# Optimization experiments

Hardware: AMD Instinct MI355X
Metric: run time of the kernel (lower is better)

The kernel has to match this reference:

```python
import jax, jax.numpy as jnp
import numpy as np

N = 4194304  # number of curve segments


def setup_inputs() -> dict:
    key = jax.random.key(0)
    k1, k2, k3, k4 = jax.random.split(key, 4)
    # small per-step turning angles (radians)
    vec = 0.001 * jax.random.normal(k1, (N,), dtype=jnp.float32)
    vec2 = 0.001 * jax.random.normal(k2, (N,), dtype=jnp.float32)
    the0 = jnp.asarray([np.pi / 6.0], dtype=jnp.float32)
    the02 = jnp.asarray([np.pi + np.arcsin(1.0 / 7.0)], dtype=jnp.float32)
    PS = jnp.zeros((1, 2), dtype=jnp.float32)
    PE = jnp.asarray([[100.0, 0.0]], dtype=jnp.float32)
    dl = jnp.asarray([0.001], dtype=jnp.float32)
    return {"vec": vec, "vec2": vec2, "the0": the0, "the02": the02,
            "PS": PS, "PE": PE, "dl": dl}


def _curve(start, the0, vec, dl):
    # Per-step rotation matvec recurrence pre_i = R(vec_i) @ pre_{i-1},
    # pre_0 = dl * R(the0) @ [1, 0]. Rotations compose additively, so the
    # recurrence is exactly cumulative angles + cumsum of step vectors.
    theta = the0 + jnp.cumsum(vec)                      # [n]
    steps = dl[0] * jnp.stack([jnp.cos(theta), jnp.sin(theta)], axis=-1)  # [n, 2]
    path = start[-1] + jnp.cumsum(steps, axis=0)        # [n, 2]
    return jnp.concatenate([start, path], axis=0)       # [n+1, 2]


def reference(vec, vec2, the0, the02, PS, PE, dl):
    P = _curve(PS, the0, vec, dl)
    P2 = _curve(PE, the02, vec2, dl)
    return (P, P2)
```

## Files before the change

kernel.cpp:

```cpp
#include <hip/hip_runtime.h>

#define NSEG   4194304
#define BLOCK  256
#define ITEMS  16
#define TILE   (BLOCK * ITEMS)
#define NTILES (NSEG / TILE)
#define WAVES  (BLOCK / 64)

static_assert(NSEG % TILE == 0, "tile must divide N");

__device__ __forceinline__ void combineSeg(float aT, float aC, float aS,
                                           float bT, float bC, float bS,
                                           float& oT, float& oC, float& oS) {
    float s, c;
    __sincosf(aT, &s, &c);
    oT = aT + bT;
    oC = aC + c * bC - s * bS;
    oS = aS + s * bC + c * bS;
}

__global__ __launch_bounds__(BLOCK) void k_tilesum(
        const float* __restrict__ vec, const float* __restrict__ vec2,
        float4* __restrict__ part) {
    const int c = blockIdx.y;
    const int b = blockIdx.x;
    const int t = threadIdx.x;
    const int lane = t & 63, wave = t >> 6;
    const float* __restrict__ v = c ? vec2 : vec;

    __shared__ float sW[WAVES], sRC[WAVES], sRS[WAVES];

    const float4* __restrict__ p =
        reinterpret_cast<const float4*>(v + (size_t)b * TILE) +
        (size_t)t * (ITEMS / 4);
    float vals[ITEMS];
#pragma unroll
    for (int q = 0; q < ITEMS / 4; ++q) {
        float4 a = p[q];
        vals[q * 4 + 0] = a.x; vals[q * 4 + 1] = a.y;
        vals[q * 4 + 2] = a.z; vals[q * 4 + 3] = a.w;
    }
    float tsum = 0.f;
#pragma unroll
    for (int k = 0; k < ITEMS; ++k) tsum += vals[k];

    float incl = tsum;
#pragma unroll
    for (int d = 1; d < 64; d <<= 1) {
        float o = __shfl_up(incl, d, 64);
        if (lane >= d) incl += o;
    }
    if (lane == 63) sW[wave] = incl;
    __syncthreads();
    float wpre = 0.f, tot = 0.f;
#pragma unroll
    for (int w = 0; w < WAVES; ++w) {
        float x = sW[w];
        if (w < wave) wpre += x;
        tot += x;
    }
    const float excl = wpre + incl - tsum;

    float run = excl, C = 0.f, S = 0.f;
#pragma unroll
    for (int k = 0; k < ITEMS; ++k) {
        run += vals[k];
        float sn, cs;
        __sincosf(run, &sn, &cs);
        C += cs; S += sn;
    }
#pragma unroll
    for (int d = 32; d > 0; d >>= 1) {
        C += __shfl_down(C, d, 64);
        S += __shfl_down(S, d, 64);
    }
    if (lane == 0) { sRC[wave] = C; sRS[wave] = S; }
    __syncthreads();
    if (t == 0) {
        float Ct = 0.f, St = 0.f;
#pragma unroll
        for (int w = 0; w < WAVES; ++w) { Ct += sRC[w]; St += sRS[w]; }
        part[c * NTILES + b] = make_float4(tot, Ct, St, 0.f);
    }
}

__global__ __launch_bounds__(BLOCK, 4) void k_emit(
        const float* __restrict__ vec, const float* __restrict__ vec2,
        const float* __restrict__ the0, const float* __restrict__ the02,
        const float* __restrict__ PS, const float* __restrict__ PE,
        const float* __restrict__ dl,
        const float4* __restrict__ part, float* __restrict__ out) {
    const int b = blockIdx.x;
    const int c = blockIdx.y;
    const int t = threadIdx.x;
    const int lane = t & 63, wave = t >> 6;
    const float* __restrict__ v = c ? vec2 : vec;

    __shared__ float sMT[WAVES], sMC[WAVES], sMS[WAVES];
    __shared__ float sPre[3];
    __shared__ float sW[WAVES], sWx[WAVES], sWy[WAVES];
    __shared__ float smX[128 * 17], smY[128 * 17];

    {
        const float4* __restrict__ pp = part + (size_t)c * NTILES;
        float aT[4], aC[4], aS[4];
        float T = 0.f, C = 0.f, S = 0.f;
#pragma unroll
        for (int j = 0; j < 4; ++j) {
            float4 d4 = pp[t * 4 + j];
            aT[j] = d4.x; aC[j] = d4.y; aS[j] = d4.z;
            combineSeg(T, C, S, aT[j], aC[j], aS[j], T, C, S);
        }
        float iT = T, iC = C, iS = S;
#pragma unroll
        for (int d = 1; d < 64; d <<= 1) {
            float oT = __shfl_up(iT, d, 64);
            float oC = __shfl_up(iC, d, 64);
            float oS = __shfl_up(iS, d, 64);
            if (lane >= d) combineSeg(oT, oC, oS, iT, iC, iS, iT, iC, iS);
        }
        float pT = __shfl_up(iT, 1, 64);
        float pC = __shfl_up(iC, 1, 64);
        float pS = __shfl_up(iS, 1, 64);
        float eT = (lane == 0) ? 0.f : pT;
        float eC = (lane == 0) ? 0.f : pC;
        float eS = (lane == 0) ? 0.f : pS;
        if (lane == 63) { sMT[wave] = iT; sMC[wave] = iC; sMS[wave] = iS; }
        __syncthreads();
        float wT = 0.f, wC = 0.f, wS = 0.f;
#pragma unroll
        for (int w = 0; w < WAVES; ++w) {
            if (w < wave) combineSeg(wT, wC, wS, sMT[w], sMC[w], sMS[w], wT, wC, wS);
        }
        float xT, xC, xS;
        combineSeg(wT, wC, wS, eT, eC, eS, xT, xC, xS);

        if (b == 0) {
            if (t == 0) { sPre[0] = 0.f; sPre[1] = 0.f; sPre[2] = 0.f; }
        } else {
            const int q = (b - 1) >> 2;
            if (t == q) {
                float PT = xT, PC = xC, PZ = xS;
                const int m = (b - 1) & 3;
                for (int j = 0; j <= m; ++j)
                    combineSeg(PT, PC, PZ, aT[j], aC[j], aS[j], PT, PC, PZ);
                sPre[0] = PT; sPre[1] = PC; sPre[2] = PZ;
            }
        }
        __syncthreads();
    }

    const float t0 = c ? the02[0] : the0[0];
    const float sx = c ? PE[0] : PS[0];
    const float sy = c ? PE[1] : PS[1];
    const float dlv = dl[0];
    float s0, c0;
    __sincosf(t0, &s0, &c0);
    const float thPre = t0 + sPre[0];
    const float pxB = sx + dlv * (c0 * sPre[1] - s0 * sPre[2]);
    const float pyB = sy + dlv * (s0 * sPre[1] + c0 * sPre[2]);

    const float4* __restrict__ p =
        reinterpret_cast<const float4*>(v + (size_t)b * TILE) +
        (size_t)t * (ITEMS / 4);
    float vals[ITEMS];
#pragma unroll
    for (int q = 0; q < ITEMS / 4; ++q) {
        float4 a = p[q];
        vals[q * 4 + 0] = a.x; vals[q * 4 + 1] = a.y;
        vals[q * 4 + 2] = a.z; vals[q * 4 + 3] = a.w;
    }
    float tsum = 0.f;
#pragma unroll
    for (int k = 0; k < ITEMS; ++k) tsum += vals[k];

    float incl = tsum;
#pragma unroll
    for (int d = 1; d < 64; d <<= 1) {
        float o = __shfl_up(incl, d, 64);
        if (lane >= d) incl += o;
    }
    if (lane == 63) sW[wave] = incl;
    __syncthreads();
    float wpre = 0.f;
#pragma unroll
    for (int w = 0; w < WAVES; ++w) {
        float x = sW[w];
        if (w < wave) wpre += x;
    }
    const float angExcl = wpre + incl - tsum;

    const float base = thPre + angExcl;
    float cs[ITEMS], sn[ITEMS];
    float run2 = base, sxs = 0.f, sys = 0.f;
#pragma unroll
    for (int k = 0; k < ITEMS; ++k) {
        run2 += vals[k];
        __sincosf(run2, &sn[k], &cs[k]);
        sxs += cs[k]; sys += sn[k];
    }

    float ix = sxs, iy = sys;
#pragma unroll
    for (int d = 1; d < 64; d <<= 1) {
        float ox = __shfl_up(ix, d, 64);
        float oy = __shfl_up(iy, d, 64);
        if (lane >= d) { ix += ox; iy += oy; }
    }
    if (lane == 63) { sWx[wave] = ix; sWy[wave] = iy; }
    __syncthreads();
    float wpx = 0.f, wpy = 0.f;
#pragma unroll
    for (int w = 0; w < WAVES; ++w) {
        if (w < wave) { wpx += sWx[w]; wpy += sWy[w]; }
    }
    const float ex = wpx + ix - sxs;
    const float ey = wpy + iy - sys;

    float px = pxB + dlv * ex;
    float py = pyB + dlv * ey;

    float2* __restrict__ o2 =
        reinterpret_cast<float2*>(out) + (size_t)c * (NSEG + 1);
    const int halfId = t >> 7;
    const int row = t & 127;

#pragma unroll
    for (int h = 0; h < 2; ++h) {
        __syncthreads();
        if (halfId == h) {
            float qx = px, qy = py;
#pragma unroll
            for (int k = 0; k < ITEMS; ++k) {
                qx += dlv * cs[k];
                qy += dlv * sn[k];
                smX[row * 17 + k] = qx;
                smY[row * 17 + k] = qy;
            }
        }
        __syncthreads();
        const size_t eBase = (size_t)b * TILE + (size_t)h * 2048 + 1;
#pragma unroll
        for (int r = 0; r < 8; ++r) {
            const int e = r * 256 + t;
            const float xx = smX[(e >> 4) * 17 + (e & 15)];
            const float yy = smY[(e >> 4) * 17 + (e & 15)];
            o2[eBase + e] = make_float2(xx, yy);
        }
    }
    if (b == 0 && t == 0) {
        o2[0] = make_float2(sx, sy);
    }
}

extern "C" void kernel_launch(void* const* d_in, const int* in_sizes, int n_in,
                              void* d_out, int out_size, void* d_ws, size_t ws_size,
                              hipStream_t stream) {
    const float* vec   = (const float*)d_in[0];
    const float* vec2  = (const float*)d_in[1];
    const float* the0  = (const float*)d_in[2];
    const float* the02 = (const float*)d_in[3];
    const float* PS    = (const float*)d_in[4];
    const float* PE    = (const float*)d_in[5];
    const float* dl    = (const float*)d_in[6];
    float* out = (float*)d_out;
    float4* part = (float4*)d_ws;

    dim3 grid(NTILES, 2);
    k_tilesum<<<grid, BLOCK, 0, stream>>>(vec, vec2, part);
    k_emit<<<grid, BLOCK, 0, stream>>>(vec, vec2, the0, the02, PS, PE, dl,
                                       part, out);
}
```

Baseline: 111.2 us.

## Stride per-thread chunks across tile and store float4 points directly without LDS staging

Each thread now handles four strided groups of four consecutive elements, each read as one coalesced float4, instead of sixteen contiguous elements. Both kernels run a block scan per group, carrying running totals between groups. In the emit kernel this lets each thread write its points straight to global memory as two float4 stores, which removes the shared-memory transpose buffers and their extra barriers. The cost is four times as many wave shuffle scans and block barriers per tile. The second curve's output base is only 8-byte aligned, so its float4 stores rely on the hardware tolerating unaligned wide stores.

```diff
diff --git a/kernel.cpp b/kernel.cpp
--- a/kernel.cpp
+++ b/kernel.cpp
@@ -2,12 +2,13 @@
 
 #define NSEG   4194304
 #define BLOCK  256
-#define ITEMS  16
-#define TILE   (BLOCK * ITEMS)
+#define TILE   4096
+#define CHUNK  1024
+#define NCHUNK 4
 #define NTILES (NSEG / TILE)
 #define WAVES  (BLOCK / 64)
 
-static_assert(NSEG % TILE == 0, "tile must divide N");
+static_assert(NTILES * TILE == NSEG, "tiling must cover N");
 
 __device__ __forceinline__ void combineSeg(float aT, float aC, float aS,
                                            float bT, float bC, float bS,
@@ -28,59 +29,55 @@
     const int lane = t & 63, wave = t >> 6;
     const float* __restrict__ v = c ? vec2 : vec;
 
-    __shared__ float sW[WAVES], sRC[WAVES], sRS[WAVES];
+    __shared__ float sW[NCHUNK][WAVES];
+    __shared__ float sRC[WAVES], sRS[WAVES];
 
     const float4* __restrict__ p =
-        reinterpret_cast<const float4*>(v + (size_t)b * TILE) +
-        (size_t)t * (ITEMS / 4);
-    float vals[ITEMS];
-#pragma unroll
-    for (int q = 0; q < ITEMS / 4; ++q) {
-        float4 a = p[q];
-        vals[q * 4 + 0] = a.x; vals[q * 4 + 1] = a.y;
-        vals[q * 4 + 2] = a.z; vals[q * 4 + 3] = a.w;
-    }
-    float tsum = 0.f;
-#pragma unroll
-    for (int k = 0; k < ITEMS; ++k) tsum += vals[k];
-
-    float incl = tsum;
-#pragma unroll
-    for (int d = 1; d < 64; d <<= 1) {
-        float o = __shfl_up(incl, d, 64);
-        if (lane >= d) incl += o;
-    }
-    if (lane == 63) sW[wave] = incl;
-    __syncthreads();
-    float wpre = 0.f, tot = 0.f;
-#pragma unroll
-    for (int w = 0; w < WAVES; ++w) {
-        float x = sW[w];
-        if (w < wave) wpre += x;
-        tot += x;
-    }
-    const float excl = wpre + incl - tsum;
-
-    float run = excl, C = 0.f, S = 0.f;
-#pragma unroll
-    for (int k = 0; k < ITEMS; ++k) {
-        run += vals[k];
+        reinterpret_cast<const float4*>(v + (size_t)b * TILE);
+    float4 a[NCHUNK];
+#pragma unroll
+    for (int g = 0; g < NCHUNK; ++g) a[g] = p[g * (CHUNK / 4) + t];
+
+    float runT = 0.f, accC = 0.f, accS = 0.f;
+#pragma unroll
+    for (int g = 0; g < NCHUNK; ++g) {
+        const float v0 = a[g].x, v1 = a[g].y, v2 = a[g].z, v3 = a[g].w;
+        float s4 = v0 + v1 + v2 + v3;
+        float incl = s4;
+#pragma unroll
+        for (int d = 1; d < 64; d <<= 1) {
+            float o = __shfl_up(incl, d, 64);
+            if (lane >= d) incl += o;
+        }
+        if (lane == 63) sW[g][wave] = incl;
+        __syncthreads();
+        float wpre = 0.f, tot = 0.f;
+#pragma unroll
+        for (int w = 0; w < WAVES; ++w) {
+            float x = sW[g][w];
+            if (w < wave) wpre += x;
+            tot += x;
+        }
+        float run = runT + wpre + incl - s4;
         float sn, cs;
-        __sincosf(run, &sn, &cs);
-        C += cs; S += sn;
+        run += v0; __sincosf(run, &sn, &cs); accC += cs; accS += sn;
+        run += v1; __sincosf(run, &sn, &cs); accC += cs; accS += sn;
+        run += v2; __sincosf(run, &sn, &cs); accC += cs; accS += sn;
+        run += v3; __sincosf(run, &sn, &cs); accC += cs; accS += sn;
+        runT += tot;
     }
 #pragma unroll
     for (int d = 32; d > 0; d >>= 1) {
-        C += __shfl_down(C, d, 64);
-        S += __shfl_down(S, d, 64);
-    }
-    if (lane == 0) { sRC[wave] = C; sRS[wave] = S; }
+        accC += __shfl_down(accC, d, 64);
+        accS += __shfl_down(accS, d, 64);
+    }
+    if (lane == 0) { sRC[wave] = accC; sRS[wave] = accS; }
     __syncthreads();
     if (t == 0) {
         float Ct = 0.f, St = 0.f;
 #pragma unroll
         for (int w = 0; w < WAVES; ++w) { Ct += sRC[w]; St += sRS[w]; }
-        part[c * NTILES + b] = make_float4(tot, Ct, St, 0.f);
+        part[c * NTILES + b] = make_float4(runT, Ct, St, 0.f);
     }
 }
 
@@ -98,8 +95,14 @@
 
     __shared__ float sMT[WAVES], sMC[WAVES], sMS[WAVES];
     __shared__ float sPre[3];
-    __shared__ float sW[WAVES], sWx[WAVES], sWy[WAVES];
-    __shared__ float smX[128 * 17], smY[128 * 17];
+    __shared__ float sW1[NCHUNK][WAVES];
+    __shared__ float sWx[NCHUNK][WAVES], sWy[NCHUNK][WAVES];
+
+    const float4* __restrict__ p =
+        reinterpret_cast<const float4*>(v + (size_t)b * TILE);
+    float4 a[NCHUNK];
+#pragma unroll
+    for (int g = 0; g < NCHUNK; ++g) a[g] = p[g * (CHUNK / 4) + t];
 
     {
         const float4* __restrict__ pp = part + (size_t)c * NTILES;
@@ -160,96 +163,69 @@
     const float pxB = sx + dlv * (c0 * sPre[1] - s0 * sPre[2]);
     const float pyB = sy + dlv * (s0 * sPre[1] + c0 * sPre[2]);
 
-    const float4* __restrict__ p =
-        reinterpret_cast<const float4*>(v + (size_t)b * TILE) +
-        (size_t)t * (ITEMS / 4);
-    float vals[ITEMS];
-#pragma unroll
-    for (int q = 0; q < ITEMS / 4; ++q) {
-        float4 a = p[q];
-        vals[q * 4 + 0] = a.x; vals[q * 4 + 1] = a.y;
-        vals[q * 4 + 2] = a.z; vals[q * 4 + 3] = a.w;
-    }
-    float tsum = 0.f;
-#pragma unroll
-    for (int k = 0; k < ITEMS; ++k) tsum += vals[k];
-
-    float incl = tsum;
-#pragma unroll
-    for (int d = 1; d < 64; d <<= 1) {
-        float o = __shfl_up(incl, d, 64);
-        if (lane >= d) incl += o;
-    }
-    if (lane == 63) sW[wave] = incl;
-    __syncthreads();
-    float wpre = 0.f;
-#pragma unroll
-    for (int w = 0; w < WAVES; ++w) {
-        float x = sW[w];
-        if (w < wave) wpre += x;
-    }
-    const float angExcl = wpre + incl - tsum;
-
-    const float base = thPre + angExcl;
-    float cs[ITEMS], sn[ITEMS];
-    float run2 = base, sxs = 0.f, sys = 0.f;
-#pragma unroll
-    for (int k = 0; k < ITEMS; ++k) {
-        run2 += vals[k];
-        __sincosf(run2, &sn[k], &cs[k]);
-        sxs += cs[k]; sys += sn[k];
-    }
-
-    float ix = sxs, iy = sys;
-#pragma unroll
-    for (int d = 1; d < 64; d <<= 1) {
-        float ox = __shfl_up(ix, d, 64);
-        float oy = __shfl_up(iy, d, 64);
-        if (lane >= d) { ix += ox; iy += oy; }
-    }
-    if (lane == 63) { sWx[wave] = ix; sWy[wave] = iy; }
-    __syncthreads();
-    float wpx = 0.f, wpy = 0.f;
-#pragma unroll
-    for (int w = 0; w < WAVES; ++w) {
-        if (w < wave) { wpx += sWx[w]; wpy += sWy[w]; }
-    }
-    const float ex = wpx + ix - sxs;
-    const float ey = wpy + iy - sys;
-
-    float px = pxB + dlv * ex;
-    float py = pyB + dlv * ey;
-
-    float2* __restrict__ o2 =
-        reinterpret_cast<float2*>(out) + (size_t)c * (NSEG + 1);
-    const int halfId = t >> 7;
-    const int row = t & 127;
-
-#pragma unroll
-    for (int h = 0; h < 2; ++h) {
-        __syncthreads();
-        if (halfId == h) {
-            float qx = px, qy = py;
-#pragma unroll
-            for (int k = 0; k < ITEMS; ++k) {
-                qx += dlv * cs[k];
-                qy += dlv * sn[k];
-                smX[row * 17 + k] = qx;
-                smY[row * 17 + k] = qy;
-            }
-        }
-        __syncthreads();
-        const size_t eBase = (size_t)b * TILE + (size_t)h * 2048 + 1;
-#pragma unroll
-        for (int r = 0; r < 8; ++r) {
-            const int e = r * 256 + t;
-            const float xx = smX[(e >> 4) * 17 + (e & 15)];
-            const float yy = smY[(e >> 4) * 17 + (e & 15)];
-            o2[eBase + e] = make_float2(xx, yy);
-        }
-    }
-    if (b == 0 && t == 0) {
-        o2[0] = make_float2(sx, sy);
+    float4* __restrict__ o4 =
+        reinterpret_cast<float4*>(out + (size_t)c * (NSEG + 1) * 2);
+    float runT = 0.f, carryC = 0.f, carryS = 0.f;
+#pragma unroll
+    for (int g = 0; g < NCHUNK; ++g) {
+        const float v0 = a[g].x, v1 = a[g].y, v2 = a[g].z, v3 = a[g].w;
+        float s4 = v0 + v1 + v2 + v3;
+        float incl = s4;
+#pragma unroll
+        for (int d = 1; d < 64; d <<= 1) {
+            float o = __shfl_up(incl, d, 64);
+            if (lane >= d) incl += o;
+        }
+        if (lane == 63) sW1[g][wave] = incl;
+        __syncthreads();
+        float wpre = 0.f, totA = 0.f;
+#pragma unroll
+        for (int w = 0; w < WAVES; ++w) {
+            float x = sW1[g][w];
+            if (w < wave) wpre += x;
+            totA += x;
+        }
+        float run = thPre + runT + wpre + incl - s4;
+        float cs[4], sn[4];
+        run += v0; __sincosf(run, &sn[0], &cs[0]);
+        run += v1; __sincosf(run, &sn[1], &cs[1]);
+        run += v2; __sincosf(run, &sn[2], &cs[2]);
+        run += v3; __sincosf(run, &sn[3], &cs[3]);
+        runT += totA;
+
+        float sC4 = cs[0] + cs[1] + cs[2] + cs[3];
+        float sS4 = sn[0] + sn[1] + sn[2] + sn[3];
+        float ix = sC4, iy = sS4;
+#pragma unroll
+        for (int d = 1; d < 64; d <<= 1) {
+            float ox = __shfl_up(ix, d, 64);
+            float oy = __shfl_up(iy, d, 64);
+            if (lane >= d) { ix += ox; iy += oy; }
+        }
+        if (lane == 63) { sWx[g][wave] = ix; sWy[g][wave] = iy; }
+        __syncthreads();
+        float wpx = 0.f, wpy = 0.f, totC = 0.f, totS = 0.f;
+#pragma unroll
+        for (int w = 0; w < WAVES; ++w) {
+            float xx = sWx[g][w], yy = sWy[g][w];
+            if (w < wave) { wpx += xx; wpy += yy; }
+            totC += xx; totS += yy;
+        }
+        const float x0 = pxB + dlv * (carryC + wpx + ix - sC4);
+        const float y0 = pyB + dlv * (carryS + wpy + iy - sS4);
+        const float x1 = x0 + dlv * cs[0], y1 = y0 + dlv * sn[0];
+        const float x2 = x1 + dlv * cs[1], y2 = y1 + dlv * sn[1];
+        const float x3 = x2 + dlv * cs[2], y3 = y2 + dlv * sn[2];
+        carryC += totC; carryS += totS;
+
+        const size_t obase = ((size_t)b * TILE + (size_t)g * CHUNK) / 2 + 2 * t;
+        o4[obase + 0] = make_float4(x0, y0, x1, y1);
+        o4[obase + 1] = make_float4(x2, y2, x3, y3);
+
+        if (g == NCHUNK - 1 && b == NTILES - 1 && t == BLOCK - 1) {
+            reinterpret_cast<float2*>(o4)[NSEG] =
+                make_float2(x3 + dlv * cs[3], y3 + dlv * sn[3]);
+        }
     }
 }
 
```

Result: slower. 115.5 us (+3.9%).
